# Kernel optimization log

Hardware: AMD Instinct MI355X
Metric: run time of the kernel (lower is better)

Reference implementation:

```python
import jax, jax.numpy as jnp
import numpy as np

TEMPERATURE = 0.1
KNN = 5
NEG = -1e30   # finite stand-in for -inf: identical softmax/threshold result, NaN-safe
EPS = -1e-08  # note: the original code really adds a NEGATIVE epsilon
MASK_VAL = -1.0


def setup_inputs() -> dict:
    key = jax.random.key(0)
    k1, k2, k3, k4 = jax.random.split(key, 4)
    n_img, max_r, n_cap, max_w, d = 128, 36, 128, 32, 512
    imgs = jax.random.normal(k1, (n_img, max_r, d), dtype=jnp.float32)
    caps = jax.random.normal(k2, (n_cap, max_w, d), dtype=jnp.float32)
    img_lens = jax.random.randint(k3, (n_img,), KNN + 1, max_r + 1, dtype=jnp.int32)
    cap_lens = jax.random.randint(k4, (n_cap,), 4, max_w + 1, dtype=jnp.int32)
    # guarantee lens.max() equals the static dims (torch slices to lens.max())
    img_lens = img_lens.at[0].set(max_r)
    cap_lens = cap_lens.at[0].set(max_w)
    return {"imgs": imgs, "caps": caps, "img_lens": img_lens, "cap_lens": cap_lens}


def reference(imgs, caps, img_lens, cap_lens):
    n_img, max_r, d = imgs.shape
    n_cap, max_w, _ = caps.shape
    knn = min(KNN, max_r)

    img_valid = jnp.arange(max_r)[None, :] < img_lens[:, None]   # [n_img, max_r]
    cap_valid = jnp.arange(max_w)[None, :] < cap_lens[:, None]   # [n_cap, max_w]
    imgs = jnp.where(img_valid[..., None], imgs, 0.0)
    caps = jnp.where(cap_valid[..., None], caps, 0.0)

    # fine-grained all-pairs similarities: [n_cap, n_img, max_w, max_r]
    sims = jnp.einsum('cwd,ird->ciwr', caps, imgs) / TEMPERATURE
    mask = cap_valid[:, None, :, None] & img_valid[None, :, None, :]
    sims = jnp.where(mask, sims, NEG)

    # top-KNN threshold along region axis (== sort()[..., max_r-KNN] in torch)
    kth = jax.lax.top_k(sims, knn)[0][..., -1:]
    sims = jnp.where(sims < kth, NEG, sims)

    attn = jax.nn.softmax(sims, axis=-1)
    attn = jnp.where(mask, attn, 0.0)

    att = jnp.einsum('ciwr,ird->ciwd', attn, imgs)                # attended regions
    num = jnp.einsum('ciwd,cwd->ciw', att, caps)
    den = jnp.linalg.norm(att, axis=-1) + EPS
    out = num / den                                               # [n_cap, n_img, max_w]
    out = jnp.where(cap_valid[:, None, :], out, MASK_VAL)
    return jnp.transpose(out, (1, 0, 2))                          # [n_img, n_cap, max_w]
```

## Files before the change

### kernel.cpp

```cpp
#include <hip/hip_runtime.h>
#include <cmath>

#define N_IMG 128
#define MAX_R 36
#define N_CAP 128
#define MAX_W 32
#define DIM   512
#define NEGV  -1e30f

typedef unsigned short u16;
typedef unsigned int   u32;
typedef unsigned char  u8;
typedef __attribute__((ext_vector_type(4))) int i32x4;

#define NI_ELEMS (N_IMG * MAX_R * DIM)
#define NC_ELEMS (N_CAP * MAX_W * DIM)

#define A_CHUNK 18432
#define B_CHUNK 16384
#define BUF_BYTES 34816
#define LDS_BYTES 69632

__device__ __forceinline__ void gload_lds16(const void* g, void* l) {
    __builtin_amdgcn_global_load_lds(
        (const __attribute__((address_space(1))) void*)g,
        (__attribute__((address_space(3))) void*)l, 16, 0, 0);
}

__global__ __launch_bounds__(256) void convert_kernel(const float* __restrict__ imgs,
                                                      const float* __restrict__ caps,
                                                      u8* __restrict__ imgsT,
                                                      u8* __restrict__ capsT) {
    const size_t ni4 = NI_ELEMS / 4;
    const size_t total4 = (NI_ELEMS + NC_ELEMS) / 4;
    const size_t stride = (size_t)gridDim.x * blockDim.x;
    for (size_t p = (size_t)blockIdx.x * blockDim.x + threadIdx.x; p < total4; p += stride) {
        const bool isImg = p < ni4;
        const float4 v = isImg ? ((const float4*)imgs)[p] : ((const float4*)caps)[p - ni4];
        const int q0 = (int)rintf(fminf(fmaxf(v.x * 4096.f, -32639.f), 32639.f));
        const int q1 = (int)rintf(fminf(fmaxf(v.y * 4096.f, -32639.f), 32639.f));
        const int q2 = (int)rintf(fminf(fmaxf(v.z * 4096.f, -32639.f), 32639.f));
        const int q3 = (int)rintf(fminf(fmaxf(v.w * 4096.f, -32639.f), 32639.f));
        const int h0 = (q0 + 128) >> 8, l0 = q0 - (h0 << 8);
        const int h1 = (q1 + 128) >> 8, l1 = q1 - (h1 << 8);
        const int h2 = (q2 + 128) >> 8, l2 = q2 - (h2 << 8);
        const int h3 = (q3 + 128) >> 8, l3 = q3 - (h3 << 8);
        const u32 hw = (u32)(h0 & 255) | ((u32)(h1 & 255) << 8) |
                       ((u32)(h2 & 255) << 16) | ((u32)(h3 & 255) << 24);
        const u32 lw = (u32)(l0 & 255) | ((u32)(l1 & 255) << 8) |
                       ((u32)(l2 & 255) << 16) | ((u32)(l3 & 255) << 24);
        if (isImg) {
            const int e = (int)(p * 4);
            const int imgRow = e >> 9, k = e & 511;
            const int g = imgRow / 144;
            const int rowT = imgRow - g * 144;
            const int kb = k >> 6, k6 = k & 63;
            const int blk = (k6 >> 4) ^ ((rowT >> 1) & 3);
            const size_t off = (size_t)(g * 8 + kb) * A_CHUNK + rowT * 64 + blk * 16 + (k6 & 15);
            *(u32*)(imgsT + off) = hw;
            *(u32*)(imgsT + off + 9216) = lw;
        } else {
            const int e = (int)((p - ni4) * 4);
            const int R = e >> 9, k = e & 511;
            const int cg = R >> 7, row = R & 127;
            const int kb = k >> 6, k6 = k & 63;
            const int blk = (k6 >> 4) ^ ((row >> 1) & 3);
            const size_t off = (size_t)(cg * 8 + kb) * B_CHUNK + row * 64 + blk * 16 + (k6 & 15);
            *(u32*)(capsT + off) = hw;
            *(u32*)(capsT + off + 8192) = lw;
        }
    }
}

__global__ __launch_bounds__(256) void gram_i8_kernel(const u8* __restrict__ imgsT,
                                                      float* __restrict__ G) {
    const int i  = blockIdx.x;
    const int gg = i >> 2;
    const int m  = i & 3;
    const int t = threadIdx.x;
    const int wid = t >> 6;
    const int lane = t & 63;
    const int l15 = lane & 15;
    const int kq = lane >> 4;

    __shared__ __align__(16) u8 sT[2][2][3072];

    const u8* base = imgsT + (size_t)gg * 8 * A_CHUNK + m * 36 * 64;

    auto stage = [&](int kb, int buf) {
        const u8* hsrc = base + (size_t)kb * A_CHUNK;
        {
            const int u = t;
            if (u < 144) gload_lds16(hsrc + u * 16, &sT[buf][0][u * 16]);
            else if (u < 288) gload_lds16(hsrc + 9216 + (u - 144) * 16, &sT[buf][1][(u - 144) * 16]);
        }
        if (t < 32) {
            const int u = 112 + t;
            gload_lds16(hsrc + 9216 + u * 16, &sT[buf][1][u * 16]);
        }
    };

    i32x4 aH[3], aC[3], aL[3];
    #pragma unroll
    for (int mt = 0; mt < 3; ++mt) {
        aH[mt] = (i32x4){0,0,0,0};
        aC[mt] = (i32x4){0,0,0,0};
        aL[mt] = (i32x4){0,0,0,0};
    }

    stage(0, 0);
    __syncthreads();

    const int m18 = 18 * m;
    for (int kb = 0; kb < 8; ++kb) {
        const int buf = kb & 1;
        if (kb < 7) stage(kb + 1, buf ^ 1);
        if (wid < 3) {
            const int brow = wid * 16 + l15;
            const int bblk = kq ^ ((m18 + (brow >> 1)) & 3);
            const i32x4 bh = *(const i32x4*)&sT[buf][0][brow * 64 + bblk * 16];
            const i32x4 bl = *(const i32x4*)&sT[buf][1][brow * 64 + bblk * 16];
            #pragma unroll
            for (int mt = 0; mt < 3; ++mt) {
                const int arow = mt * 16 + l15;
                const int ablk = kq ^ ((m18 + (arow >> 1)) & 3);
                const i32x4 ah = *(const i32x4*)&sT[buf][0][arow * 64 + ablk * 16];
                const i32x4 al = *(const i32x4*)&sT[buf][1][arow * 64 + ablk * 16];
                aH[mt] = __builtin_amdgcn_mfma_i32_16x16x64_i8(ah, bh, aH[mt], 0, 0, 0);
                aC[mt] = __builtin_amdgcn_mfma_i32_16x16x64_i8(ah, bl, aC[mt], 0, 0, 0);
                aC[mt] = __builtin_amdgcn_mfma_i32_16x16x64_i8(al, bh, aC[mt], 0, 0, 0);
                aL[mt] = __builtin_amdgcn_mfma_i32_16x16x64_i8(al, bl, aL[mt], 0, 0, 0);
            }
        }
        __syncthreads();
    }

    if (wid < 3) {
        const int col = wid * 16 + l15;
        if (col < 36) {
            #pragma unroll
            for (int mt = 0; mt < 3; ++mt) {
                #pragma unroll
                for (int e = 0; e < 4; ++e) {
                    const int row = mt * 16 + kq * 4 + e;
                    if (row < 36) {
                        const float g = (float)aH[mt][e] * (1.f / 256.f)
                                      + (float)aC[mt][e] * (1.f / 65536.f)
                                      + (float)aL[mt][e] * (1.f / 16777216.f);
                        G[(size_t)i * 1296 + row * 36 + col] = g;
                    }
                }
            }
        }
    }
}

__global__ __launch_bounds__(256, 2) void vsc_mfma_kernel(const u8* __restrict__ imgsT,
                                const u8* __restrict__ capsT,
                                const int* __restrict__ img_lens,
                                const int* __restrict__ cap_lens,
                                const float* __restrict__ G,
                                float* __restrict__ out) {
    extern __shared__ __align__(16) char smem[];
    const int bid = blockIdx.x;
    const int xcd = bid & 7;
    const int r_  = bid >> 3;
    const int g   = (r_ >> 5) * 8 + xcd;
    const int cg  = r_ & 31;
    const int t = threadIdx.x;
    const int wid = t >> 6;
    const int lane = t & 63;
    const int l15 = lane & 15;
    const int kblk = lane >> 4;

    const u8* gA = imgsT + (size_t)g * 8 * A_CHUNK;
    const u8* gB = capsT + (size_t)cg * 8 * B_CHUNK;

    auto stage = [&](int kb, char* buf) {
        if (wid < 2) {
            const u8* src = gA + (size_t)kb * A_CHUNK + wid * 9216 + lane * 16;
            char* dst = buf + wid * 9216;
            #pragma unroll
            for (int jj = 0; jj < 9; ++jj)
                gload_lds16(src + jj * 1024, dst + jj * 1024);
        } else {
            const int wb = wid - 2;
            const u8* src = gB + (size_t)kb * B_CHUNK + wb * 8192 + lane * 16;
            char* dst = buf + 18432 + wb * 8192;
            #pragma unroll
            for (int jj = 0; jj < 8; ++jj)
                gload_lds16(src + jj * 1024, dst + jj * 1024);
        }
    };

    i32x4 accH[9][2], accC[9][2];
    #pragma unroll
    for (int mt = 0; mt < 9; ++mt)
        #pragma unroll
        for (int nt = 0; nt < 2; ++nt) {
            accH[mt][nt] = (i32x4){0, 0, 0, 0};
            accC[mt][nt] = (i32x4){0, 0, 0, 0};
        }

    stage(0, smem);
    __syncthreads();

    const int blk16 = (kblk ^ ((l15 >> 1) & 3)) << 4;
    const int baseA = l15 * 64 + blk16;
    const int baseB = (wid * 32 + l15) * 64 + blk16;

    for (int kb = 0; kb < 8; ++kb) {
        char* cur = smem + (size_t)(kb & 1) * BUF_BYTES;
        if (kb < 7) stage(kb + 1, smem + (size_t)((kb + 1) & 1) * BUF_BYTES);

        const i32x4 bh0 = *(const i32x4*)(cur + 18432 + baseB);
        const i32x4 bl0 = *(const i32x4*)(cur + 26624 + baseB);
        const i32x4 bh1 = *(const i32x4*)(cur + 18432 + baseB + 1024);
        const i32x4 bl1 = *(const i32x4*)(cur + 26624 + baseB + 1024);
        __builtin_amdgcn_s_setprio(1);
        #pragma unroll
        for (int mt = 0; mt < 9; ++mt) {
            const i32x4 ah = *(const i32x4*)(cur + baseA + mt * 1024);
            const i32x4 al = *(const i32x4*)(cur + 9216 + baseA + mt * 1024);
            i32x4 lt0 = (i32x4){0, 0, 0, 0};
            i32x4 lt1 = (i32x4){0, 0, 0, 0};
            lt0 = __builtin_amdgcn_mfma_i32_16x16x64_i8(al, bl0, lt0, 0, 0, 0);
            lt1 = __builtin_amdgcn_mfma_i32_16x16x64_i8(al, bl1, lt1, 0, 0, 0);
            accH[mt][0] = __builtin_amdgcn_mfma_i32_16x16x64_i8(ah, bh0, accH[mt][0], 0, 0, 0);
            accH[mt][1] = __builtin_amdgcn_mfma_i32_16x16x64_i8(ah, bh1, accH[mt][1], 0, 0, 0);
            accC[mt][0] = __builtin_amdgcn_mfma_i32_16x16x64_i8(ah, bl0, accC[mt][0], 0, 0, 0);
            accC[mt][0] = __builtin_amdgcn_mfma_i32_16x16x64_i8(al, bh0, accC[mt][0], 0, 0, 0);
            accC[mt][1] = __builtin_amdgcn_mfma_i32_16x16x64_i8(ah, bl1, accC[mt][1], 0, 0, 0);
            accC[mt][1] = __builtin_amdgcn_mfma_i32_16x16x64_i8(al, bh1, accC[mt][1], 0, 0, 0);
            #pragma unroll
            for (int e = 0; e < 4; ++e) {
                accC[mt][0][e] += lt0[e] >> 8;
                accC[mt][1][e] += lt1[e] >> 8;
            }
        }
        __builtin_amdgcn_s_setprio(0);
        __syncthreads();
    }

    float* sG = (float*)smem;
    {
        const float4* src = (const float4*)(G + (size_t)g * 4 * 1296);
        for (int idx = t; idx < 1296; idx += 256)
            ((float4*)sG)[idx] = src[idx];
    }
    __syncthreads();

    int ilen_[4];
    #pragma unroll
    for (int j = 0; j < 4; ++j) ilen_[j] = img_lens[g * 4 + j];

    #pragma unroll
    for (int nt = 0; nt < 2; ++nt) {
        const int col = wid * 32 + nt * 16 + l15;
        const int c = cg * 4 + (col >> 5);
        const int w = col & 31;
        const int clen = cap_lens[c];
        #pragma unroll
        for (int j = 0; j < 4; ++j) {
            const int mtb = (36 * j) >> 4;
            const int ilenj = ilen_[j];
            float tv0 = NEGV, tv1 = NEGV, tv2 = NEGV, tv3 = NEGV, tv4 = NEGV;
            #pragma unroll
            for (int dm = 0; dm < 3; ++dm) {
                #pragma unroll
                for (int e = 0; e < 4; ++e) {
                    const int mt = mtb + dm;
                    const int r = mt * 16 + kblk * 4 + e;
                    const int rr = r - 36 * j;
                    const float sval = (float)accH[mt][nt][e] * (10.f / 256.f)
                                     + (float)accC[mt][nt][e] * (10.f / 65536.f);
                    float v = NEGV;
                    if ((unsigned)rr < (unsigned)ilenj)
                        v = __uint_as_float((__float_as_uint(sval) & ~63u) | (u32)rr);
                    const bool c0 = v > tv0, c1 = v > tv1, c2 = v > tv2, c3 = v > tv3, c4 = v > tv4;
                    const float n4 = c4 ? (c3 ? tv3 : v) : tv4;
                    const float n3 = c3 ? (c2 ? tv2 : v) : tv3;
                    const float n2 = c2 ? (c1 ? tv1 : v) : tv2;
                    const float n1 = c1 ? (c0 ? tv0 : v) : tv1;
                    const float n0 = c0 ? v : tv0;
                    tv0 = n0; tv1 = n1; tv2 = n2; tv3 = n3; tv4 = n4;
                }
            }
            float ta[5] = {tv0, tv1, tv2, tv3, tv4};
            #pragma unroll
            for (int st = 0; st < 2; ++st) {
                const int dx = 16 << st;
                float tb[5];
                #pragma unroll
                for (int s = 0; s < 5; ++s) tb[s] = __shfl_xor(ta[s], dx);
                float na[5];
                #pragma unroll
                for (int k = 0; k < 5; ++k) {
                    float best = fmaxf(ta[k], tb[k]);
                    #pragma unroll
                    for (int i2 = 1; i2 <= k; ++i2)
                        best = fmaxf(best, fminf(ta[i2 - 1], tb[k - i2]));
                    na[k] = best;
                }
                #pragma unroll
                for (int s = 0; s < 5; ++s) ta[s] = na[s];
            }
            const float m = ta[0];
            const float p0 = 1.f;
            const float p1 = expf(ta[1] - m);
            const float p2 = expf(ta[2] - m);
            const float p3 = expf(ta[3] - m);
            const float p4 = expf(ta[4] - m);
            const float sum = p0 + p1 + p2 + p3 + p4;
            const float num = p0 * ta[0] + p1 * ta[1] + p2 * ta[2] + p3 * ta[3] + p4 * ta[4];
            const int r0 = __float_as_uint(ta[0]) & 63;
            const int r1 = __float_as_uint(ta[1]) & 63;
            const int r2 = __float_as_uint(ta[2]) & 63;
            const int r3 = __float_as_uint(ta[3]) & 63;
            const int r4 = __float_as_uint(ta[4]) & 63;
            const float* gj = sG + j * 1296;
            const float pa = (kblk == 0) ? p0 : (kblk == 1) ? p1 : (kblk == 2) ? p2 : p3;
            const int   ra = (kblk == 0) ? r0 : (kblk == 1) ? r1 : (kblk == 2) ? r2 : r3;
            const float* grow = gj + ra * 36;
            float part = pa * (p0 * grow[r0] + p1 * grow[r1] + p2 * grow[r2]
                             + p3 * grow[r3] + p4 * grow[r4]);
            if (kblk == 0) {
                const float* grow4 = gj + r4 * 36;
                part += p4 * (p0 * grow4[r0] + p1 * grow4[r1] + p2 * grow4[r2]
                            + p3 * grow4[r3] + p4 * grow4[r4]);
            }
            part += __shfl_xor(part, 16);
            part += __shfl_xor(part, 32);
            if (kblk == j) {
                float result = -1.f;
                if (w < clen) {
                    const float inv = 1.f / sum;
                    const float a_ = 0.1f * num * inv;
                    const float den = sqrtf(part) * inv + (-1e-8f);
                    result = a_ / den;
                }
                out[((size_t)(g * 4 + j) * N_CAP + c) * MAX_W + w] = result;
            }
        }
    }
}

extern "C" void kernel_launch(void* const* d_in, const int* in_sizes, int n_in,
                              void* d_out, int out_size, void* d_ws, size_t ws_size,
                              hipStream_t stream) {
    const float* imgs     = (const float*)d_in[0];
    const float* caps     = (const float*)d_in[1];
    const int*   img_lens = (const int*)d_in[2];
    const int*   cap_lens = (const int*)d_in[3];
    float* out = (float*)d_out;

    float* G  = (float*)d_ws;
    u8* imgsT = (u8*)d_ws + 663552;
    u8* capsT = imgsT + (size_t)32 * 8 * A_CHUNK;

    hipFuncSetAttribute((const void*)vsc_mfma_kernel,
                        hipFuncAttributeMaxDynamicSharedMemorySize, LDS_BYTES);

    convert_kernel<<<2048, 256, 0, stream>>>(imgs, caps, imgsT, capsT);
    gram_i8_kernel<<<N_IMG, 256, 0, stream>>>(imgsT, G);
    vsc_mfma_kernel<<<1024, 256, LDS_BYTES, stream>>>(imgsT, capsT, img_lens, cap_lens, G, out);
}
```

Measured before the change: 78.70 us.

## Load caption B fragments directly into registers, stage only images in LDS

Caption data is re-laid out in the convert kernel so that each lane's MFMA B-operand fragment is a contiguous 16-byte chunk in global memory. The main kernel then loads these fragments straight into registers with one-step-ahead prefetch instead of staging them through LDS, which halves the LDS buffer and removes the LDS reads for B. Only the image tile is still staged via global_load_lds, now spread across all four waves. The cost is more register pressure and direct global loads whose latency must be hidden by the prefetch, and the K loop is fully unrolled.

Result: slower. 131.1 us (+66.6%).

```diff
diff --git a/kernel.cpp b/kernel.cpp
--- a/kernel.cpp
+++ b/kernel.cpp
@@ -18,8 +18,8 @@
 
 #define A_CHUNK 18432
 #define B_CHUNK 16384
-#define BUF_BYTES 34816
-#define LDS_BYTES 69632
+#define BUF_BYTES 18432
+#define LDS_BYTES 36864
 
 __device__ __forceinline__ void gload_lds16(const void* g, void* l) {
     __builtin_amdgcn_global_load_lds(
@@ -62,12 +62,14 @@
         } else {
             const int e = (int)((p - ni4) * 4);
             const int R = e >> 9, k = e & 511;
-            const int cg = R >> 7, row = R & 127;
+            const int c = R >> 5, w = R & 31;
+            const int cg = c >> 2, q = c & 3;
             const int kb = k >> 6, k6 = k & 63;
-            const int blk = (k6 >> 4) ^ ((row >> 1) & 3);
-            const size_t off = (size_t)(cg * 8 + kb) * B_CHUNK + row * 64 + blk * 16 + (k6 & 15);
+            const int lane = ((k6 >> 4) << 4) | (w & 15);
+            const size_t off = (size_t)(cg * 8 + kb) * B_CHUNK + q * 4096
+                             + ((w >> 4) << 10) + lane * 16 + (k6 & 15);
             *(u32*)(capsT + off) = hw;
-            *(u32*)(capsT + off + 8192) = lw;
+            *(u32*)(capsT + off + 2048) = lw;
         }
     }
 }
@@ -174,22 +176,18 @@
     const int kblk = lane >> 4;
 
     const u8* gA = imgsT + (size_t)g * 8 * A_CHUNK;
-    const u8* gB = capsT + (size_t)cg * 8 * B_CHUNK;
-
-    auto stage = [&](int kb, char* buf) {
-        if (wid < 2) {
-            const u8* src = gA + (size_t)kb * A_CHUNK + wid * 9216 + lane * 16;
-            char* dst = buf + wid * 9216;
-            #pragma unroll
-            for (int jj = 0; jj < 9; ++jj)
-                gload_lds16(src + jj * 1024, dst + jj * 1024);
-        } else {
-            const int wb = wid - 2;
-            const u8* src = gB + (size_t)kb * B_CHUNK + wb * 8192 + lane * 16;
-            char* dst = buf + 18432 + wb * 8192;
-            #pragma unroll
-            for (int jj = 0; jj < 8; ++jj)
-                gload_lds16(src + jj * 1024, dst + jj * 1024);
+    const u8* gB = capsT + (size_t)cg * 8 * B_CHUNK + wid * 4096 + lane * 16;
+
+    auto stageA = [&](int kb, char* buf) {
+        const u8* src = gA + (size_t)kb * A_CHUNK;
+        #pragma unroll
+        for (int j = 0; j < 4; ++j) {
+            const int u = t + j * 256;
+            gload_lds16(src + u * 16, buf + u * 16);
+        }
+        if (t < 128) {
+            const int u = 1024 + t;
+            gload_lds16(src + u * 16, buf + u * 16);
         }
     };
 
@@ -202,21 +200,30 @@
             accC[mt][nt] = (i32x4){0, 0, 0, 0};
         }
 
-    stage(0, smem);
+    stageA(0, smem);
+    i32x4 bh0c = *(const i32x4*)(gB + 0);
+    i32x4 bh1c = *(const i32x4*)(gB + 1024);
+    i32x4 bl0c = *(const i32x4*)(gB + 2048);
+    i32x4 bl1c = *(const i32x4*)(gB + 3072);
     __syncthreads();
 
     const int blk16 = (kblk ^ ((l15 >> 1) & 3)) << 4;
     const int baseA = l15 * 64 + blk16;
-    const int baseB = (wid * 32 + l15) * 64 + blk16;
-
+
+    #pragma unroll
     for (int kb = 0; kb < 8; ++kb) {
         char* cur = smem + (size_t)(kb & 1) * BUF_BYTES;
-        if (kb < 7) stage(kb + 1, smem + (size_t)((kb + 1) & 1) * BUF_BYTES);
-
-        const i32x4 bh0 = *(const i32x4*)(cur + 18432 + baseB);
-        const i32x4 bl0 = *(const i32x4*)(cur + 26624 + baseB);
-        const i32x4 bh1 = *(const i32x4*)(cur + 18432 + baseB + 1024);
-        const i32x4 bl1 = *(const i32x4*)(cur + 26624 + baseB + 1024);
+        if (kb < 7) stageA(kb + 1, smem + (size_t)((kb + 1) & 1) * BUF_BYTES);
+
+        i32x4 bh0n, bh1n, bl0n, bl1n;
+        if (kb < 7) {
+            const u8* nb = gB + (size_t)(kb + 1) * B_CHUNK;
+            bh0n = *(const i32x4*)(nb + 0);
+            bh1n = *(const i32x4*)(nb + 1024);
+            bl0n = *(const i32x4*)(nb + 2048);
+            bl1n = *(const i32x4*)(nb + 3072);
+        }
+
         __builtin_amdgcn_s_setprio(1);
         #pragma unroll
         for (int mt = 0; mt < 9; ++mt) {
@@ -224,14 +231,14 @@
             const i32x4 al = *(const i32x4*)(cur + 9216 + baseA + mt * 1024);
             i32x4 lt0 = (i32x4){0, 0, 0, 0};
             i32x4 lt1 = (i32x4){0, 0, 0, 0};
-            lt0 = __builtin_amdgcn_mfma_i32_16x16x64_i8(al, bl0, lt0, 0, 0, 0);
-            lt1 = __builtin_amdgcn_mfma_i32_16x16x64_i8(al, bl1, lt1, 0, 0, 0);
-            accH[mt][0] = __builtin_amdgcn_mfma_i32_16x16x64_i8(ah, bh0, accH[mt][0], 0, 0, 0);
-            accH[mt][1] = __builtin_amdgcn_mfma_i32_16x16x64_i8(ah, bh1, accH[mt][1], 0, 0, 0);
-            accC[mt][0] = __builtin_amdgcn_mfma_i32_16x16x64_i8(ah, bl0, accC[mt][0], 0, 0, 0);
-            accC[mt][0] = __builtin_amdgcn_mfma_i32_16x16x64_i8(al, bh0, accC[mt][0], 0, 0, 0);
-            accC[mt][1] = __builtin_amdgcn_mfma_i32_16x16x64_i8(ah, bl1, accC[mt][1], 0, 0, 0);
-            accC[mt][1] = __builtin_amdgcn_mfma_i32_16x16x64_i8(al, bh1, accC[mt][1], 0, 0, 0);
+            lt0 = __builtin_amdgcn_mfma_i32_16x16x64_i8(al, bl0c, lt0, 0, 0, 0);
+            lt1 = __builtin_amdgcn_mfma_i32_16x16x64_i8(al, bl1c, lt1, 0, 0, 0);
+            accH[mt][0] = __builtin_amdgcn_mfma_i32_16x16x64_i8(ah, bh0c, accH[mt][0], 0, 0, 0);
+            accH[mt][1] = __builtin_amdgcn_mfma_i32_16x16x64_i8(ah, bh1c, accH[mt][1], 0, 0, 0);
+            accC[mt][0] = __builtin_amdgcn_mfma_i32_16x16x64_i8(ah, bl0c, accC[mt][0], 0, 0, 0);
+            accC[mt][0] = __builtin_amdgcn_mfma_i32_16x16x64_i8(al, bh0c, accC[mt][0], 0, 0, 0);
+            accC[mt][1] = __builtin_amdgcn_mfma_i32_16x16x64_i8(ah, bl1c, accC[mt][1], 0, 0, 0);
+            accC[mt][1] = __builtin_amdgcn_mfma_i32_16x16x64_i8(al, bh1c, accC[mt][1], 0, 0, 0);
             #pragma unroll
             for (int e = 0; e < 4; ++e) {
                 accC[mt][0][e] += lt0[e] >> 8;
@@ -240,6 +247,8 @@
         }
         __builtin_amdgcn_s_setprio(0);
         __syncthreads();
+
+        if (kb < 7) { bh0c = bh0n; bh1c = bh1n; bl0c = bl0n; bl1c = bl1n; }
     }
 
     float* sG = (float*)smem;
```
